# Performance work log

Measured on AMD Instinct MI355X. Metric: run time of the kernel, lower is better.

## Reference

```python
import jax, jax.numpy as jnp
import numpy as np

DIM1, DIM2, NUM_ANS = 1024, 1024, 1000
B, T = 64, 128


def setup_inputs() -> dict:
    key = jax.random.key(0)
    ks = jax.random.split(key, 12)
    H, D_IN = DIM1, DIM1 + DIM2
    s = 0.02
    return {
        "data1": jax.random.normal(ks[0], (B, T, DIM1), dtype=jnp.float32),
        "data2": jax.random.normal(ks[1], (B, T, DIM2), dtype=jnp.float32),
        # layer-1 LSTM (input D_IN -> hidden H), PyTorch gate order i,f,g,o
        "W_ih1": jax.random.normal(ks[2], (4 * H, D_IN), dtype=jnp.float32) * s,
        "W_hh1": jax.random.normal(ks[3], (4 * H, H), dtype=jnp.float32) * s,
        "b1": jax.random.normal(ks[4], (4 * H,), dtype=jnp.float32) * s,
        # layer-2 LSTM (H -> H)
        "W_ih2": jax.random.normal(ks[5], (4 * H, H), dtype=jnp.float32) * s,
        "W_hh2": jax.random.normal(ks[6], (4 * H, H), dtype=jnp.float32) * s,
        "b2": jax.random.normal(ks[7], (4 * H,), dtype=jnp.float32) * s,
        # predict MLP: dim1 -> dim1//4 -> num_ans
        "Wp1": jax.random.normal(ks[8], (DIM1, DIM1 // 4), dtype=jnp.float32) * s,
        "bp1": jnp.zeros((DIM1 // 4,), dtype=jnp.float32),
        "Wp2": jax.random.normal(ks[9], (DIM1 // 4, NUM_ANS), dtype=jnp.float32) * s,
        "bp2": jnp.zeros((NUM_ANS,), dtype=jnp.float32),
    }


def _lstm_cell(x, h, c, Wih, Whh, b):
    gates = x @ Wih.T + h @ Whh.T + b  # [B, 4H]
    i, f, g, o = jnp.split(gates, 4, axis=-1)
    c_new = jax.nn.sigmoid(f) * c + jax.nn.sigmoid(i) * jnp.tanh(g)
    h_new = jax.nn.sigmoid(o) * jnp.tanh(c_new)
    return h_new, c_new


def reference(data1, data2, W_ih1, W_hh1, b1, W_ih2, W_hh2, b2, Wp1, bp1, Wp2, bp2):
    joint = jnp.concatenate((data1, data2), axis=-1)  # [B, T, dim1+dim2]
    Bb = joint.shape[0]
    H = W_hh1.shape[1]
    z = jnp.zeros((Bb, H), dtype=joint.dtype)

    def step(carry, x_t):
        h1, c1, h2, c2 = carry
        h1, c1 = _lstm_cell(x_t, h1, c1, W_ih1, W_hh1, b1)
        h2, c2 = _lstm_cell(h1, h2, c2, W_ih2, W_hh2, b2)
        out_t = h2 + h1  # residual connection between layers
        return (h1, c1, h2, c2), out_t

    xs = jnp.swapaxes(joint, 0, 1)  # [T, B, D]
    _, outs = jax.lax.scan(step, (z, z, z, z), xs)
    lstm_out = jnp.swapaxes(outs, 0, 1)  # [B, T, H]

    hid = jax.nn.relu(lstm_out @ Wp1 + bp1)  # dropout is identity at inference
    logits = hid @ Wp2 + bp2  # [B, T, num_ans]
    return jax.nn.softmax(jnp.squeeze(logits), axis=-1)
```

## Files before the change

kernel.cpp:

```cpp
#include <hip/hip_runtime.h>
#include <math.h>

#define BB   64
#define TT   128
#define HH   1024
#define DIN  2048
#define G4   4096
#define MALL 8192
#define NANS 1000

typedef __attribute__((ext_vector_type(8))) short bf16x8;
typedef __attribute__((ext_vector_type(4))) float f32x4;

__device__ __forceinline__ float sigmoidf_(float x) { return 1.0f / (1.0f + expf(-x)); }

__device__ __forceinline__ unsigned short f2bf(float f) {
  unsigned u = __float_as_uint(f);
  u = (u + 0x7fff + ((u >> 16) & 1)) >> 16;
  return (unsigned short)u;
}
__device__ __forceinline__ float bf2f(unsigned short h) {
  return __uint_as_float(((unsigned)h) << 16);
}
__device__ __forceinline__ f32x4 mfma16(bf16x8 a, bf16x8 b, f32x4 c) {
  return __builtin_amdgcn_mfma_f32_16x16x32_bf16(a, b, c, 0, 0, 0);
}

__global__ __launch_bounds__(256) void concat_cast(
    const float* __restrict__ a, const float* __restrict__ b,
    unsigned short* __restrict__ o, int rshift, long total)
{
  long idx = ((long)blockIdx.x * 256 + threadIdx.x) * 4;
  if (idx >= total) return;
  int row = (int)(idx >> rshift);
  int col = (int)(idx & ((1L << rshift) - 1));
  int half = 1 << (rshift - 1);
  const float* s = (col < half) ? (a + (size_t)row * half + col)
                                : (b + (size_t)row * half + col - half);
  float4 v = *(const float4*)s;
  ushort4 ov;
  ov.x = f2bf(v.x); ov.y = f2bf(v.y); ov.z = f2bf(v.z); ov.w = f2bf(v.w);
  *(ushort4*)(o + idx) = ov;
}

__global__ __launch_bounds__(256) void cast_bf16(
    const float* __restrict__ s, unsigned short* __restrict__ o, long n)
{
  long idx = ((long)blockIdx.x * 256 + threadIdx.x) * 4;
  if (idx >= n) return;
  float4 v = *(const float4*)(s + idx);
  ushort4 ov;
  ov.x = f2bf(v.x); ov.y = f2bf(v.y); ov.z = f2bf(v.z); ov.w = f2bf(v.w);
  *(ushort4*)(o + idx) = ov;
}

__global__ __launch_bounds__(256) void cvt_wp1(
    const float* __restrict__ Wp1, unsigned short* __restrict__ o)
{
  int idx = blockIdx.x * 256 + threadIdx.x;
  int n = idx >> 10, k = idx & 1023;
  o[idx] = f2bf(Wp1[(size_t)k * 256 + n]);
}

__global__ __launch_bounds__(256) void cvt_wp2(
    const float* __restrict__ Wp2, unsigned short* __restrict__ o)
{
  int idx = blockIdx.x * 256 + threadIdx.x;
  int n = idx >> 8, k = idx & 255;
  o[idx] = f2bf(n < NANS ? Wp2[(size_t)k * NANS + n] : 0.f);
}

__global__ __launch_bounds__(256) void zero_f4(float4* __restrict__ p)
{
  p[blockIdx.x * 256 + threadIdx.x] = make_float4(0.f, 0.f, 0.f, 0.f);
}

template<int OUT_BF16, int RELU, int PERM>
__global__ __launch_bounds__(256) void mfma_gemm(
    const unsigned short* __restrict__ A,
    const unsigned short* __restrict__ W,
    const float* __restrict__ bias,
    void* __restrict__ Cout,
    int M, int N, int K, int ldc, int nvalid)
{
  __shared__ __align__(16) unsigned short As[128 * 72];
  __shared__ __align__(16) unsigned short Bs[128 * 72];
  const int t = threadIdx.x;
  const int n0 = blockIdx.x * 128, m0 = blockIdx.y * 128;
  const int w = t >> 6, lane = t & 63, lr = lane & 15, q = lane >> 4;
  const int wn = (w & 1) * 64, wm = (w >> 1) * 64;
  f32x4 acc[4][4] = {};
  for (int k0 = 0; k0 < K; k0 += 64) {
    #pragma unroll
    for (int s = 0; s < 4; s++) {
      int ci = s * 256 + t;
      int row = ci >> 3, c = ci & 7;
      bf16x8 va = *(const bf16x8*)(A + (size_t)(m0 + row) * K + k0 + c * 8);
      *(bf16x8*)(As + row * 72 + c * 8) = va;
      bf16x8 vb = *(const bf16x8*)(W + (size_t)(n0 + row) * K + k0 + c * 8);
      *(bf16x8*)(Bs + row * 72 + c * 8) = vb;
    }
    __syncthreads();
    #pragma unroll
    for (int kk = 0; kk < 2; kk++) {
      bf16x8 a[4], b[4];
      #pragma unroll
      for (int mt = 0; mt < 4; mt++)
        a[mt] = *(const bf16x8*)(As + (wm + mt * 16 + lr) * 72 + kk * 32 + q * 8);
      #pragma unroll
      for (int nt = 0; nt < 4; nt++)
        b[nt] = *(const bf16x8*)(Bs + (wn + nt * 16 + lr) * 72 + kk * 32 + q * 8);
      #pragma unroll
      for (int mt = 0; mt < 4; mt++)
        #pragma unroll
        for (int nt = 0; nt < 4; nt++)
          acc[mt][nt] = mfma16(a[mt], b[nt], acc[mt][nt]);
    }
    __syncthreads();
  }
  #pragma unroll
  for (int mt = 0; mt < 4; mt++)
    #pragma unroll
    for (int nt = 0; nt < 4; nt++)
      #pragma unroll
      for (int r = 0; r < 4; r++) {
        int row = m0 + wm + mt * 16 + q * 4 + r;
        int col = n0 + wn + nt * 16 + lr;
        if (col < nvalid) {
          float v = acc[mt][nt][r] + bias[col];
          if (RELU) v = fmaxf(v, 0.f);
          if (PERM) row = ((row & 127) << 6) | (row >> 7);
          if (OUT_BF16)
            ((unsigned short*)Cout)[(size_t)row * ldc + col] = f2bf(v);
          else
            ((float*)Cout)[(size_t)row * ldc + col] = v;
        }
      }
}

__global__ __launch_bounds__(512) void lstm_phase(
    const unsigned short* __restrict__ Whh1b,
    const unsigned short* __restrict__ W2cat,
    const unsigned short* __restrict__ gxb,
    const float* __restrict__ b2,
    int p,
    unsigned short* __restrict__ hbuf,
    float* __restrict__ c1, float* __restrict__ c2,
    unsigned short* __restrict__ lob)
{
  __shared__ float red[4][64][34];
  const int t = threadIdx.x;
  const int w = t >> 6, lane = t & 63, lr = lane & 15, q = lane >> 4;
  const int kq = w & 3, rh = w >> 2;
  const bool isA = (blockIdx.x < 128);
  const int j0 = (isA ? blockIdx.x : blockIdx.x - 128) * 8;
  const int g0 = lr >> 2, u0 = lr & 3;
  const int cm = t >> 3, cu = t & 7, ju = j0 + cu;
  const unsigned short* hprev = hbuf + (size_t)((p + 1) & 1) * 131072;
  unsigned short*       hc    = hbuf + (size_t)(p & 1) * 131072;

  if (isA) {
    if (p == TT) return;
    const unsigned short* gp = gxb + ((size_t)(p << 6) + cm) * 4096 + ju;
    unsigned short gi = gp[0], gf = gp[1024], gg2 = gp[2048], go = gp[3072];
    {
      const int kof = kq * 256 + q * 8;
      const unsigned short* wp0 =
          Whh1b + (size_t)(g0 * 1024 + j0 + u0) * 1024 + kof;
      const unsigned short* wp1 = wp0 + 4 * 1024;
      const unsigned short* hb  = hprev + (size_t)(rh * 32 + lr) * 2048 + kof;
      f32x4 acc[2][2] = {};
      #pragma unroll
      for (int ks = 0; ks < 8; ks++) {
        bf16x8 b0 = *(const bf16x8*)(wp0 + ks * 32);
        bf16x8 b1 = *(const bf16x8*)(wp1 + ks * 32);
        #pragma unroll
        for (int mt = 0; mt < 2; mt++) {
          bf16x8 af = *(const bf16x8*)(hb + (size_t)(mt * 16) * 2048 + ks * 32);
          acc[mt][0] = mfma16(af, b0, acc[mt][0]);
          acc[mt][1] = mfma16(af, b1, acc[mt][1]);
        }
      }
      #pragma unroll
      for (int mt = 0; mt < 2; mt++)
        #pragma unroll
        for (int r = 0; r < 4; r++) {
          red[kq][rh * 32 + mt * 16 + q * 4 + r][lr]      = acc[mt][0][r];
          red[kq][rh * 32 + mt * 16 + q * 4 + r][17 + lr] = acc[mt][1][r];
        }
    }
    __syncthreads();
    const int cb = (cu >> 2) * 17 + (cu & 3);
    float s[4];
    #pragma unroll
    for (int gg = 0; gg < 4; gg++)
      s[gg] = red[0][cm][cb + gg * 4] + red[1][cm][cb + gg * 4]
            + red[2][cm][cb + gg * 4] + red[3][cm][cb + gg * 4];
    s[0] += bf2f(gi); s[1] += bf2f(gf); s[2] += bf2f(gg2); s[3] += bf2f(go);
    float i_ = sigmoidf_(s[0]), f_ = sigmoidf_(s[1]);
    float g_ = tanhf(s[2]), o_ = sigmoidf_(s[3]);
    float c = f_ * c1[cm * 1024 + ju] + i_ * g_;
    c1[cm * 1024 + ju] = c;
    hc[(size_t)cm * 2048 + ju] = f2bf(o_ * tanhf(c));
  } else {
    if (p == 0) return;
    {
      const int kof = kq * 512 + q * 8;
      const unsigned short* wp0 =
          W2cat + (size_t)(g0 * 1024 + j0 + u0) * 2048 + kof;
      const unsigned short* wp1 = wp0 + 4 * 2048;
      const unsigned short* hbase = (kq < 2) ? hprev : hc;
      const unsigned short* hb = hbase + (size_t)(rh * 32 + lr) * 2048 + kof;
      f32x4 acc[2][2] = {};
      #pragma unroll
      for (int ks = 0; ks < 16; ks++) {
        bf16x8 b0 = *(const bf16x8*)(wp0 + ks * 32);
        bf16x8 b1 = *(const bf16x8*)(wp1 + ks * 32);
        #pragma unroll
        for (int mt = 0; mt < 2; mt++) {
          bf16x8 af = *(const bf16x8*)(hb + (size_t)(mt * 16) * 2048 + ks * 32);
          acc[mt][0] = mfma16(af, b0, acc[mt][0]);
          acc[mt][1] = mfma16(af, b1, acc[mt][1]);
        }
      }
      #pragma unroll
      for (int mt = 0; mt < 2; mt++)
        #pragma unroll
        for (int r = 0; r < 4; r++) {
          red[kq][rh * 32 + mt * 16 + q * 4 + r][lr]      = acc[mt][0][r];
          red[kq][rh * 32 + mt * 16 + q * 4 + r][17 + lr] = acc[mt][1][r];
        }
    }
    __syncthreads();
    const int cb = (cu >> 2) * 17 + (cu & 3);
    float s[4];
    #pragma unroll
    for (int gg = 0; gg < 4; gg++)
      s[gg] = red[0][cm][cb + gg * 4] + red[1][cm][cb + gg * 4]
            + red[2][cm][cb + gg * 4] + red[3][cm][cb + gg * 4]
            + b2[gg * 1024 + ju];
    float i_ = sigmoidf_(s[0]), f_ = sigmoidf_(s[1]);
    float g_ = tanhf(s[2]), o_ = sigmoidf_(s[3]);
    float c = f_ * c2[cm * 1024 + ju] + i_ * g_;
    c2[cm * 1024 + ju] = c;
    float h2v = o_ * tanhf(c);
    ((unsigned short*)hprev)[(size_t)cm * 2048 + 1024 + ju] = f2bf(h2v);
    float h1v = bf2f(hprev[(size_t)cm * 2048 + ju]);
    lob[((size_t)(cm << 7) + (p - 1)) * 1024 + ju] = f2bf(h1v + h2v);
  }
}

__global__ __launch_bounds__(256) void softmax_k(float* __restrict__ out)
{
  __shared__ float smax[4];
  __shared__ float ssum[4];
  const int m = blockIdx.x;
  const int t = threadIdx.x;
  const int lane = t & 63, wid = t >> 6;
  const bool act = (t < 250);
  float x[4] = {0.f, 0.f, 0.f, 0.f};
  if (act) *(float4*)x = *(const float4*)(out + (size_t)m * NANS + t * 4);
  float v = act ? fmaxf(fmaxf(x[0], x[1]), fmaxf(x[2], x[3])) : -1e30f;
  #pragma unroll
  for (int o = 32; o > 0; o >>= 1) v = fmaxf(v, __shfl_down(v, o));
  if (lane == 0) smax[wid] = v;
  __syncthreads();
  const float mx = fmaxf(fmaxf(smax[0], smax[1]), fmaxf(smax[2], smax[3]));
  float e[4] = {0.f, 0.f, 0.f, 0.f};
  float s = 0.f;
  if (act) {
    e[0] = expf(x[0] - mx); e[1] = expf(x[1] - mx);
    e[2] = expf(x[2] - mx); e[3] = expf(x[3] - mx);
    s = (e[0] + e[1]) + (e[2] + e[3]);
  }
  #pragma unroll
  for (int o = 32; o > 0; o >>= 1) s += __shfl_down(s, o);
  if (lane == 0) ssum[wid] = s;
  __syncthreads();
  const float inv = 1.0f / (((ssum[0] + ssum[1]) + (ssum[2] + ssum[3])));
  if (act) {
    float4 o4 = make_float4(e[0] * inv, e[1] * inv, e[2] * inv, e[3] * inv);
    *(float4*)(out + (size_t)m * NANS + t * 4) = o4;
  }
}

extern "C" void kernel_launch(void* const* d_in, const int* in_sizes, int n_in,
                              void* d_out, int out_size, void* d_ws, size_t ws_size,
                              hipStream_t stream)
{
  const float* d1   = (const float*)d_in[0];
  const float* d2   = (const float*)d_in[1];
  const float* Wih1 = (const float*)d_in[2];
  const float* Whh1 = (const float*)d_in[3];
  const float* b1   = (const float*)d_in[4];
  const float* Wih2 = (const float*)d_in[5];
  const float* Whh2 = (const float*)d_in[6];
  const float* b2   = (const float*)d_in[7];
  const float* Wp1  = (const float*)d_in[8];
  const float* bp1  = (const float*)d_in[9];
  const float* Wp2  = (const float*)d_in[10];
  const float* bp2  = (const float*)d_in[11];
  float* out = (float*)d_out;

  unsigned char* p = (unsigned char*)d_ws;
  unsigned short* gxb   = (unsigned short*)p;  p += 67108864;
  unsigned short* jb    = (unsigned short*)p;  p += 33554432;
  unsigned short* Wb1   = (unsigned short*)p;  p += 16777216;
  unsigned short* W2cat = (unsigned short*)p;  p += 16777216;
  unsigned short* Whh1b = (unsigned short*)p;  p += 8388608;
  unsigned short* lob   = (unsigned short*)p;  p += 16777216;
  unsigned short* hidb  = (unsigned short*)p;  p += 4194304;
  unsigned short* Wp1t  = (unsigned short*)p;  p += 524288;
  unsigned short* Wp2t  = (unsigned short*)p;  p += 524288;
  unsigned short* hbuf  = (unsigned short*)p;  p += 524288;
  float*          c1    = (float*)p;           p += 262144;
  float*          c2    = (float*)p;           p += 262144;
  if (ws_size < (size_t)(p - (unsigned char*)d_ws)) return;

  concat_cast<<<16384, 256, 0, stream>>>(d1, d2, jb, 11, 16777216L);
  cast_bf16<<<8192, 256, 0, stream>>>(Wih1, Wb1, 8388608L);
  cast_bf16<<<4096, 256, 0, stream>>>(Whh1, Whh1b, 4194304L);
  concat_cast<<<8192, 256, 0, stream>>>(Wih2, Whh2, W2cat, 11, 8388608L);
  cvt_wp1<<<1024, 256, 0, stream>>>(Wp1, Wp1t);
  cvt_wp2<<<1024, 256, 0, stream>>>(Wp2, Wp2t);
  zero_f4<<<256, 256, 0, stream>>>((float4*)hbuf);

  mfma_gemm<1, 0, 1><<<dim3(32, 64), 256, 0, stream>>>(
      jb, Wb1, b1, gxb, MALL, G4, DIN, G4, G4);

  for (int ph = 0; ph <= TT; ph++)
    lstm_phase<<<256, 512, 0, stream>>>(Whh1b, W2cat, gxb, b2, ph,
                                        hbuf, c1, c2, lob);

  mfma_gemm<1, 1, 0><<<dim3(2, 64), 256, 0, stream>>>(
      lob, Wp1t, bp1, hidb, MALL, 256, 1024, 256, 256);
  mfma_gemm<0, 0, 0><<<dim3(8, 64), 256, 0, stream>>>(
      hidb, Wp2t, bp2, out, MALL, 1024, 256, NANS, NANS);
  softmax_k<<<MALL, 256, 0, stream>>>(out);
}
```

Baseline: 2.784 ms.

## Fuse per-timestep LSTM launches into one persistent kernel with grid barrier

```diff
diff --git a/kernel.cpp b/kernel.cpp
--- a/kernel.cpp
+++ b/kernel.cpp
@@ -24,6 +24,20 @@
 }
 __device__ __forceinline__ f32x4 mfma16(bf16x8 a, bf16x8 b, f32x4 c) {
   return __builtin_amdgcn_mfma_f32_16x16x32_bf16(a, b, c, 0, 0, 0);
+}
+
+__device__ __forceinline__ bf16x8 ld_h16(const unsigned short* p) {
+  union { unsigned long long u[2]; bf16x8 v; } r;
+  unsigned long long* q = (unsigned long long*)p;
+  r.u[0] = __hip_atomic_load(q,     __ATOMIC_RELAXED, __HIP_MEMORY_SCOPE_AGENT);
+  r.u[1] = __hip_atomic_load(q + 1, __ATOMIC_RELAXED, __HIP_MEMORY_SCOPE_AGENT);
+  return r.v;
+}
+__device__ __forceinline__ unsigned short ld_h2(const unsigned short* p) {
+  return __hip_atomic_load((unsigned short*)p, __ATOMIC_RELAXED, __HIP_MEMORY_SCOPE_AGENT);
+}
+__device__ __forceinline__ void st_h2(unsigned short* p, unsigned short v) {
+  __hip_atomic_store(p, v, __ATOMIC_RELAXED, __HIP_MEMORY_SCOPE_AGENT);
 }
 
 __global__ __launch_bounds__(256) void concat_cast(
@@ -70,9 +84,11 @@
   o[idx] = f2bf(n < NANS ? Wp2[(size_t)k * NANS + n] : 0.f);
 }
 
-__global__ __launch_bounds__(256) void zero_f4(float4* __restrict__ p)
+__global__ __launch_bounds__(256) void zero_hb(
+    float4* __restrict__ p, unsigned int* __restrict__ bar)
 {
   p[blockIdx.x * 256 + threadIdx.x] = make_float4(0.f, 0.f, 0.f, 0.f);
+  if (blockIdx.x == 0 && threadIdx.x == 0) *bar = 0u;
 }
 
 template<int OUT_BF16, int RELU, int PERM>
@@ -138,15 +154,14 @@
       }
 }
 
-__global__ __launch_bounds__(512) void lstm_phase(
+__global__ __launch_bounds__(512) void lstm_persist(
     const unsigned short* __restrict__ Whh1b,
     const unsigned short* __restrict__ W2cat,
     const unsigned short* __restrict__ gxb,
     const float* __restrict__ b2,
-    int p,
     unsigned short* __restrict__ hbuf,
-    float* __restrict__ c1, float* __restrict__ c2,
-    unsigned short* __restrict__ lob)
+    unsigned short* __restrict__ lob,
+    unsigned int* __restrict__ bar)
 {
   __shared__ float red[4][64][34];
   const int t = threadIdx.x;
@@ -156,97 +171,117 @@
   const int j0 = (isA ? blockIdx.x : blockIdx.x - 128) * 8;
   const int g0 = lr >> 2, u0 = lr & 3;
   const int cm = t >> 3, cu = t & 7, ju = j0 + cu;
-  const unsigned short* hprev = hbuf + (size_t)((p + 1) & 1) * 131072;
-  unsigned short*       hc    = hbuf + (size_t)(p & 1) * 131072;
-
-  if (isA) {
-    if (p == TT) return;
-    const unsigned short* gp = gxb + ((size_t)(p << 6) + cm) * 4096 + ju;
-    unsigned short gi = gp[0], gf = gp[1024], gg2 = gp[2048], go = gp[3072];
-    {
-      const int kof = kq * 256 + q * 8;
-      const unsigned short* wp0 =
-          Whh1b + (size_t)(g0 * 1024 + j0 + u0) * 1024 + kof;
-      const unsigned short* wp1 = wp0 + 4 * 1024;
-      const unsigned short* hb  = hprev + (size_t)(rh * 32 + lr) * 2048 + kof;
-      f32x4 acc[2][2] = {};
-      #pragma unroll
-      for (int ks = 0; ks < 8; ks++) {
-        bf16x8 b0 = *(const bf16x8*)(wp0 + ks * 32);
-        bf16x8 b1 = *(const bf16x8*)(wp1 + ks * 32);
+  const int cb = (cu >> 2) * 17 + (cu & 3);
+  float creg = 0.f;
+
+  const unsigned short* wpA0 =
+      Whh1b + (size_t)(g0 * 1024 + j0 + u0) * 1024 + kq * 256 + q * 8;
+  const unsigned short* wpA1 = wpA0 + 4 * 1024;
+  const unsigned short* wpB0 =
+      W2cat + (size_t)(g0 * 1024 + j0 + u0) * 2048 + kq * 512 + q * 8;
+  const unsigned short* wpB1 = wpB0 + 4 * 2048;
+
+  for (int p = 0; p <= TT; p++) {
+    const unsigned short* hprev = hbuf + (size_t)((p + 1) & 1) * 131072;
+    unsigned short*       hc    = hbuf + (size_t)(p & 1) * 131072;
+
+    if (isA) {
+      if (p < TT) {
+        const unsigned short* gp = gxb + ((size_t)(p << 6) + cm) * 4096 + ju;
+        unsigned short gi = gp[0], gf = gp[1024], gg2 = gp[2048], go = gp[3072];
+        {
+          const int kof = kq * 256 + q * 8;
+          const unsigned short* hb = hprev + (size_t)(rh * 32 + lr) * 2048 + kof;
+          f32x4 acc[2][2] = {};
+          #pragma unroll
+          for (int ks = 0; ks < 8; ks++) {
+            bf16x8 b0 = *(const bf16x8*)(wpA0 + ks * 32);
+            bf16x8 b1 = *(const bf16x8*)(wpA1 + ks * 32);
+            #pragma unroll
+            for (int mt = 0; mt < 2; mt++) {
+              bf16x8 af = ld_h16(hb + (size_t)(mt * 16) * 2048 + ks * 32);
+              acc[mt][0] = mfma16(af, b0, acc[mt][0]);
+              acc[mt][1] = mfma16(af, b1, acc[mt][1]);
+            }
+          }
+          #pragma unroll
+          for (int mt = 0; mt < 2; mt++)
+            #pragma unroll
+            for (int r = 0; r < 4; r++) {
+              red[kq][rh * 32 + mt * 16 + q * 4 + r][lr]      = acc[mt][0][r];
+              red[kq][rh * 32 + mt * 16 + q * 4 + r][17 + lr] = acc[mt][1][r];
+            }
+        }
+        __syncthreads();
+        float s[4];
         #pragma unroll
-        for (int mt = 0; mt < 2; mt++) {
-          bf16x8 af = *(const bf16x8*)(hb + (size_t)(mt * 16) * 2048 + ks * 32);
-          acc[mt][0] = mfma16(af, b0, acc[mt][0]);
-          acc[mt][1] = mfma16(af, b1, acc[mt][1]);
+        for (int gg = 0; gg < 4; gg++)
+          s[gg] = red[0][cm][cb + gg * 4] + red[1][cm][cb + gg * 4]
+                + red[2][cm][cb + gg * 4] + red[3][cm][cb + gg * 4];
+        s[0] += bf2f(gi); s[1] += bf2f(gf); s[2] += bf2f(gg2); s[3] += bf2f(go);
+        float i_ = sigmoidf_(s[0]), f_ = sigmoidf_(s[1]);
+        float g_ = tanhf(s[2]), o_ = sigmoidf_(s[3]);
+        float c = f_ * creg + i_ * g_;
+        creg = c;
+        st_h2(hc + (size_t)cm * 2048 + ju, f2bf(o_ * tanhf(c)));
+      }
+    } else {
+      if (p > 0) {
+        {
+          const int kof = kq * 512 + q * 8;
+          const unsigned short* hbase = (kq < 2) ? hprev : hc;
+          const unsigned short* hb = hbase + (size_t)(rh * 32 + lr) * 2048 + kof;
+          f32x4 acc[2][2] = {};
+          #pragma unroll
+          for (int ks = 0; ks < 16; ks++) {
+            bf16x8 b0 = *(const bf16x8*)(wpB0 + ks * 32);
+            bf16x8 b1 = *(const bf16x8*)(wpB1 + ks * 32);
+            #pragma unroll
+            for (int mt = 0; mt < 2; mt++) {
+              bf16x8 af = ld_h16(hb + (size_t)(mt * 16) * 2048 + ks * 32);
+              acc[mt][0] = mfma16(af, b0, acc[mt][0]);
+              acc[mt][1] = mfma16(af, b1, acc[mt][1]);
+            }
+          }
+          #pragma unroll
+          for (int mt = 0; mt < 2; mt++)
+            #pragma unroll
+            for (int r = 0; r < 4; r++) {
+              red[kq][rh * 32 + mt * 16 + q * 4 + r][lr]      = acc[mt][0][r];
+              red[kq][rh * 32 + mt * 16 + q * 4 + r][17 + lr] = acc[mt][1][r];
+            }
+        }
+        __syncthreads();
+        float s[4];
+        #pragma unroll
+        for (int gg = 0; gg < 4; gg++)
+          s[gg] = red[0][cm][cb + gg * 4] + red[1][cm][cb + gg * 4]
+                + red[2][cm][cb + gg * 4] + red[3][cm][cb + gg * 4]
+                + b2[gg * 1024 + ju];
+        float i_ = sigmoidf_(s[0]), f_ = sigmoidf_(s[1]);
+        float g_ = tanhf(s[2]), o_ = sigmoidf_(s[3]);
+        float c = f_ * creg + i_ * g_;
+        creg = c;
+        float h2v = o_ * tanhf(c);
+        st_h2((unsigned short*)hprev + (size_t)cm * 2048 + 1024 + ju, f2bf(h2v));
+        float h1v = bf2f(ld_h2(hprev + (size_t)cm * 2048 + ju));
+        lob[((size_t)(cm << 7) + (p - 1)) * 1024 + ju] = f2bf(h1v + h2v);
+      }
+    }
+
+    if (p < TT) {
+      __syncthreads();
+      if (t == 0) {
+        __hip_atomic_fetch_add(bar, 1u, __ATOMIC_RELAXED, __HIP_MEMORY_SCOPE_AGENT);
+        const unsigned tgt = 256u * (unsigned)(p + 1);
+        unsigned iters = 0;
+        while (__hip_atomic_load(bar, __ATOMIC_RELAXED, __HIP_MEMORY_SCOPE_AGENT) < tgt) {
+          __builtin_amdgcn_s_sleep(4);
+          if (++iters > 100000000u) break;
         }
       }
-      #pragma unroll
-      for (int mt = 0; mt < 2; mt++)
-        #pragma unroll
-        for (int r = 0; r < 4; r++) {
-          red[kq][rh * 32 + mt * 16 + q * 4 + r][lr]      = acc[mt][0][r];
-          red[kq][rh * 32 + mt * 16 + q * 4 + r][17 + lr] = acc[mt][1][r];
-        }
+      __syncthreads();
     }
-    __syncthreads();
-    const int cb = (cu >> 2) * 17 + (cu & 3);
-    float s[4];
-    #pragma unroll
-    for (int gg = 0; gg < 4; gg++)
-      s[gg] = red[0][cm][cb + gg * 4] + red[1][cm][cb + gg * 4]
-            + red[2][cm][cb + gg * 4] + red[3][cm][cb + gg * 4];
-    s[0] += bf2f(gi); s[1] += bf2f(gf); s[2] += bf2f(gg2); s[3] += bf2f(go);
-    float i_ = sigmoidf_(s[0]), f_ = sigmoidf_(s[1]);
-    float g_ = tanhf(s[2]), o_ = sigmoidf_(s[3]);
-    float c = f_ * c1[cm * 1024 + ju] + i_ * g_;
-    c1[cm * 1024 + ju] = c;
-    hc[(size_t)cm * 2048 + ju] = f2bf(o_ * tanhf(c));
-  } else {
-    if (p == 0) return;
-    {
-      const int kof = kq * 512 + q * 8;
-      const unsigned short* wp0 =
-          W2cat + (size_t)(g0 * 1024 + j0 + u0) * 2048 + kof;
-      const unsigned short* wp1 = wp0 + 4 * 2048;
-      const unsigned short* hbase = (kq < 2) ? hprev : hc;
-      const unsigned short* hb = hbase + (size_t)(rh * 32 + lr) * 2048 + kof;
-      f32x4 acc[2][2] = {};
-      #pragma unroll
-      for (int ks = 0; ks < 16; ks++) {
-        bf16x8 b0 = *(const bf16x8*)(wp0 + ks * 32);
-        bf16x8 b1 = *(const bf16x8*)(wp1 + ks * 32);
-        #pragma unroll
-        for (int mt = 0; mt < 2; mt++) {
-          bf16x8 af = *(const bf16x8*)(hb + (size_t)(mt * 16) * 2048 + ks * 32);
-          acc[mt][0] = mfma16(af, b0, acc[mt][0]);
-          acc[mt][1] = mfma16(af, b1, acc[mt][1]);
-        }
-      }
-      #pragma unroll
-      for (int mt = 0; mt < 2; mt++)
-        #pragma unroll
-        for (int r = 0; r < 4; r++) {
-          red[kq][rh * 32 + mt * 16 + q * 4 + r][lr]      = acc[mt][0][r];
-          red[kq][rh * 32 + mt * 16 + q * 4 + r][17 + lr] = acc[mt][1][r];
-        }
-    }
-    __syncthreads();
-    const int cb = (cu >> 2) * 17 + (cu & 3);
-    float s[4];
-    #pragma unroll
-    for (int gg = 0; gg < 4; gg++)
-      s[gg] = red[0][cm][cb + gg * 4] + red[1][cm][cb + gg * 4]
-            + red[2][cm][cb + gg * 4] + red[3][cm][cb + gg * 4]
-            + b2[gg * 1024 + ju];
-    float i_ = sigmoidf_(s[0]), f_ = sigmoidf_(s[1]);
-    float g_ = tanhf(s[2]), o_ = sigmoidf_(s[3]);
-    float c = f_ * c2[cm * 1024 + ju] + i_ * g_;
-    c2[cm * 1024 + ju] = c;
-    float h2v = o_ * tanhf(c);
-    ((unsigned short*)hprev)[(size_t)cm * 2048 + 1024 + ju] = f2bf(h2v);
-    float h1v = bf2f(hprev[(size_t)cm * 2048 + ju]);
-    lob[((size_t)(cm << 7) + (p - 1)) * 1024 + ju] = f2bf(h1v + h2v);
   }
 }
 
@@ -313,8 +348,7 @@
   unsigned short* Wp1t  = (unsigned short*)p;  p += 524288;
   unsigned short* Wp2t  = (unsigned short*)p;  p += 524288;
   unsigned short* hbuf  = (unsigned short*)p;  p += 524288;
-  float*          c1    = (float*)p;           p += 262144;
-  float*          c2    = (float*)p;           p += 262144;
+  unsigned int*   bar   = (unsigned int*)p;    p += 256;
   if (ws_size < (size_t)(p - (unsigned char*)d_ws)) return;
 
   concat_cast<<<16384, 256, 0, stream>>>(d1, d2, jb, 11, 16777216L);
@@ -323,14 +357,12 @@
   concat_cast<<<8192, 256, 0, stream>>>(Wih2, Whh2, W2cat, 11, 8388608L);
   cvt_wp1<<<1024, 256, 0, stream>>>(Wp1, Wp1t);
   cvt_wp2<<<1024, 256, 0, stream>>>(Wp2, Wp2t);
-  zero_f4<<<256, 256, 0, stream>>>((float4*)hbuf);
+  zero_hb<<<128, 256, 0, stream>>>((float4*)hbuf, bar);
 
   mfma_gemm<1, 0, 1><<<dim3(32, 64), 256, 0, stream>>>(
       jb, Wb1, b1, gxb, MALL, G4, DIN, G4, G4);
 
-  for (int ph = 0; ph <= TT; ph++)
-    lstm_phase<<<256, 512, 0, stream>>>(Whh1b, W2cat, gxb, b2, ph,
-                                        hbuf, c1, c2, lob);
+  lstm_persist<<<256, 512, 0, stream>>>(Whh1b, W2cat, gxb, b2, hbuf, lob, bar);
 
   mfma_gemm<1, 1, 0><<<dim3(2, 64), 256, 0, stream>>>(
       lob, Wp1t, bp1, hidb, MALL, 256, 1024, 256, 256);
```

Measured after the change: 4.143 ms. 1.49x slower.
